# Performance work log

Hardware: AMD Instinct MI355X
Metric: run time of the kernel (lower is better)

## Reference

```python
import jax, jax.numpy as jnp
import numpy as np

N_NODES = 50000
N_EDGES = 800000
IN_DIM, HID, OUT = 128, 64, 64
NUM_REL = 2
LN_EPS = 1e-5


def setup_inputs() -> dict:
    key = jax.random.key(0)
    ks = jax.random.split(key, 16)
    inp = {
        "x": jax.random.normal(ks[0], (N_NODES, IN_DIM), dtype=jnp.float32),
        "edge_index": jax.random.randint(ks[1], (2, N_EDGES), 0, N_NODES, dtype=jnp.int64),
        "edge_type": jax.random.randint(ks[2], (N_EDGES,), 0, NUM_REL, dtype=jnp.int64),
        # layer 1 params (RGCNConv input->hidden + LayerNorm)
        "W1": jax.random.normal(ks[3], (NUM_REL, IN_DIM, HID), dtype=jnp.float32) * 0.05,
        "root1": jax.random.normal(ks[4], (IN_DIM, HID), dtype=jnp.float32) * 0.05,
        "b1": jnp.zeros((HID,), dtype=jnp.float32),
        "g1": jnp.ones((HID,), dtype=jnp.float32),
        "beta1": jnp.zeros((HID,), dtype=jnp.float32),
        # layer 2 params (RGCNConv hidden->output + LayerNorm)
        "W2": jax.random.normal(ks[5], (NUM_REL, HID, OUT), dtype=jnp.float32) * 0.05,
        "root2": jax.random.normal(ks[6], (HID, OUT), dtype=jnp.float32) * 0.05,
        "b2": jnp.zeros((OUT,), dtype=jnp.float32),
        "g2": jnp.ones((OUT,), dtype=jnp.float32),
        "beta2": jnp.zeros((OUT,), dtype=jnp.float32),
    }
    return inp


def rgcn_conv(x, W, root, bias, src, dst, edge_type, num_nodes):
    # PyG RGCNConv (aggr='mean'): out = x @ root + bias + sum_r mean_{j in N_r(i)} x_j @ W_r
    out = x @ root + bias
    for r in range(NUM_REL):
        mask = (edge_type == r).astype(x.dtype)        # [E]
        proj = x @ W[r]                                 # [N, out]
        msg = proj[src] * mask[:, None]                 # [E, out] gather + mask
        agg = jax.ops.segment_sum(msg, dst, num_segments=num_nodes)   # scatter-add
        cnt = jax.ops.segment_sum(mask, dst, num_segments=num_nodes)  # per-relation in-degree
        out = out + agg / jnp.maximum(cnt, 1.0)[:, None]
    return out


def layer_norm(x, g, b):
    mu = jnp.mean(x, axis=-1, keepdims=True)
    var = jnp.mean(jnp.square(x - mu), axis=-1, keepdims=True)
    return (x - mu) * jax.lax.rsqrt(var + LN_EPS) * g + b


def reference(x, edge_index, edge_type, W1, root1, b1, g1, beta1, W2, root2, b2, g2, beta2):
    src, dst = edge_index[0], edge_index[1]
    h = rgcn_conv(x, W1, root1, b1, src, dst, edge_type, x.shape[0])
    h = layer_norm(h, g1, beta1)
    h = jax.nn.gelu(h, approximate=False)  # dropout is identity in eval mode
    h = rgcn_conv(h, W2, root2, b2, src, dst, edge_type, x.shape[0])
    h = layer_norm(h, g2, beta2)
    return h
```

## Files before the change

### kernel.cpp

```cpp
#include <hip/hip_runtime.h>
#include <hip/hip_bf16.h>
#include <math.h>

#define IN_DIM 128
#define HID 64
#define NREL 2

using f32x4 = __attribute__((ext_vector_type(4))) float;
using s16x8 = __attribute__((ext_vector_type(8))) short;

__device__ __forceinline__ short f2bf(float f) {
    unsigned u = __float_as_uint(f);
    unsigned r = (u + 0x7fffu + ((u >> 16) & 1u)) >> 16;
    return (short)r;
}
__device__ __forceinline__ float bf2f(short b) {
    return __uint_as_float(((unsigned)(unsigned short)b) << 16);
}

__global__ void zero_ints(int* p, int n) {
    int i = blockIdx.x * blockDim.x + threadIdx.x;
    if (i < n) p[i] = 0;
}

__global__ void count_edges(const int* __restrict__ et, const int* __restrict__ dst,
                            int* __restrict__ cnt, int E, int N) {
    int e = blockIdx.x * blockDim.x + threadIdx.x;
    if (e < E) {
        atomicAdd(&cnt[et[e] * N + dst[e]], 1);
    }
}

#define SCAN_T 256
#define SCAN_I 4
__global__ void scan_phase1(const int* __restrict__ in, int* __restrict__ excl,
                            int* __restrict__ bsum, int n) {
    __shared__ int sdata[SCAN_T];
    int b = blockIdx.x;
    int t = threadIdx.x;
    int base = b * SCAN_T * SCAN_I;
    int v[SCAN_I];
    int s = 0;
#pragma unroll
    for (int i = 0; i < SCAN_I; ++i) {
        int idx = base + t * SCAN_I + i;
        v[i] = (idx < n) ? in[idx] : 0;
        s += v[i];
    }
    sdata[t] = s;
    __syncthreads();
    for (int off = 1; off < SCAN_T; off <<= 1) {
        int x = (t >= off) ? sdata[t - off] : 0;
        __syncthreads();
        sdata[t] += x;
        __syncthreads();
    }
    int run = sdata[t] - s;
    if (bsum && t == SCAN_T - 1) bsum[b] = sdata[SCAN_T - 1];
#pragma unroll
    for (int i = 0; i < SCAN_I; ++i) {
        int idx = base + t * SCAN_I + i;
        if (idx < n) excl[idx] = run;
        run += v[i];
    }
}

__global__ void scan_phase3(const int* __restrict__ excl, const int* __restrict__ boff,
                            int* __restrict__ rowptr, int* __restrict__ cursor,
                            int n, int total) {
    int i = blockIdx.x * blockDim.x + threadIdx.x;
    if (i < n) {
        int v = excl[i] + boff[i / (SCAN_T * SCAN_I)];
        rowptr[i] = v;
        cursor[i] = v;
    }
    if (i == 0) rowptr[n] = total;
}

__global__ void fill_edges(const int* __restrict__ et, const int* __restrict__ src,
                           const int* __restrict__ dst, int* __restrict__ cursor,
                           int* __restrict__ col, int E, int N) {
    int e = blockIdx.x * blockDim.x + threadIdx.x;
    if (e < E) {
        int slot = atomicAdd(&cursor[et[e] * N + dst[e]], 1);
        col[slot] = src[e];
    }
}

__device__ __forceinline__ void repack_one(const float* Wa, const float* Wb,
                                           const float* Wr, short* Wf, int T,
                                           int idx) {
    int g = idx >> 9;
    int r = idx & 511;
    int lane = r >> 3;
    int j = r & 7;
    int part = g & 1;
    int ct = g >> 1;
    int t = ct % T;
    int c = ct / T;
    int col = c * 16 + (lane & 15);
    int k = t * 32 + ((lane >> 4) << 3) + j;
    const float* Wg = (col < 64) ? Wa : (col < 128) ? Wb : Wr;
    float v = Wg[(size_t)k * 64 + (col & 63)];
    short hi = f2bf(v);
    Wf[idx] = part ? f2bf(v - bf2f(hi)) : hi;
}

__global__ void repack_w_frag(const float* __restrict__ W1,
                              const float* __restrict__ root1,
                              const float* __restrict__ W2,
                              const float* __restrict__ root2,
                              short* __restrict__ Wf1, short* __restrict__ Wf2) {
    const int L1 = 12 * 4 * 2 * 512;
    const int L2 = 12 * 2 * 2 * 512;
    int tid = blockIdx.x * blockDim.x + threadIdx.x;
    if (tid < L1) {
        repack_one(W1, W1 + (size_t)IN_DIM * 64, root1, Wf1, 4, tid);
    } else if (tid < L1 + L2) {
        repack_one(W2, W2 + (size_t)HID * 64, root2, Wf2, 2, tid - L1);
    }
}

template <int K>
__global__ __launch_bounds__(256) void gemm_mfma(
    const float* __restrict__ X, const short* __restrict__ Wf,
    float* __restrict__ PA, float* __restrict__ PB, float* __restrict__ PR,
    int M) {
    constexpr int T = K / 32;
    const int lane = threadIdx.x & 63;
    const int wid = threadIdx.x >> 6;
    const int row0 = blockIdx.x * 32 + (wid >> 1) * 16;
    const int cbase = (wid & 1) * 6;

    int arow = row0 + (lane & 15);
    if (arow > M - 1) arow = M - 1;
    const float* xr = X + (size_t)arow * K + ((lane >> 4) << 3);
    const s16x8* WfV = (const s16x8*)Wf;

    float4 xa[T][2];
#pragma unroll
    for (int t = 0; t < T; ++t) {
        xa[t][0] = *reinterpret_cast<const float4*>(xr + t * 32);
        xa[t][1] = *reinterpret_cast<const float4*>(xr + t * 32 + 4);
    }
    s16x8 ah[T], al[T];
#pragma unroll
    for (int t = 0; t < T; ++t) {
        const float av[8] = {xa[t][0].x, xa[t][0].y, xa[t][0].z, xa[t][0].w,
                             xa[t][1].x, xa[t][1].y, xa[t][1].z, xa[t][1].w};
#pragma unroll
        for (int j = 0; j < 8; ++j) {
            short h = f2bf(av[j]);
            ah[t][j] = h;
            al[t][j] = f2bf(av[j] - bf2f(h));
        }
    }

    f32x4 acc[6];
#pragma unroll
    for (int c = 0; c < 6; ++c) acc[c] = (f32x4){0.f, 0.f, 0.f, 0.f};

    s16x8 bhA[T], blA[T], bhB[T], blB[T];

#define LOADB(H, L, CG)                                                       \
    {                                                                         \
        _Pragma("unroll") for (int t = 0; t < T; ++t) {                       \
            H[t] = WfV[(size_t)(((CG) * T + t) * 2 + 0) * 64 + lane];         \
            L[t] = WfV[(size_t)(((CG) * T + t) * 2 + 1) * 64 + lane];         \
        }                                                                     \
    }
#define DOMFMA(H, L, CI)                                                      \
    {                                                                         \
        _Pragma("unroll") for (int t = 0; t < T; ++t) {                       \
            acc[CI] = __builtin_amdgcn_mfma_f32_16x16x32_bf16(ah[t], H[t],    \
                                                              acc[CI], 0, 0, 0); \
            acc[CI] = __builtin_amdgcn_mfma_f32_16x16x32_bf16(al[t], H[t],    \
                                                              acc[CI], 0, 0, 0); \
            acc[CI] = __builtin_amdgcn_mfma_f32_16x16x32_bf16(ah[t], L[t],    \
                                                              acc[CI], 0, 0, 0); \
        }                                                                     \
    }

    LOADB(bhA, blA, cbase + 0);
    LOADB(bhB, blB, cbase + 1);
    DOMFMA(bhA, blA, 0);
    LOADB(bhA, blA, cbase + 2);
    DOMFMA(bhB, blB, 1);
    LOADB(bhB, blB, cbase + 3);
    DOMFMA(bhA, blA, 2);
    LOADB(bhA, blA, cbase + 4);
    DOMFMA(bhB, blB, 3);
    LOADB(bhB, blB, cbase + 5);
    DOMFMA(bhA, blA, 4);
    DOMFMA(bhB, blB, 5);

#undef LOADB
#undef DOMFMA

    const int drow = row0 + ((lane >> 4) << 2);
    const int dcol = lane & 15;
#pragma unroll
    for (int ci = 0; ci < 6; ++ci) {
        const int cg = cbase + ci;
        float* base = (cg < 4) ? PA : (cg < 8) ? PB : PR;
        const int cc = (cg & 3) * 16 + dcol;
#pragma unroll
        for (int q = 0; q < 4; ++q) {
            const int row = drow + q;
            if (row < M) base[(size_t)row * 64 + cc] = acc[ci][q];
        }
    }
}

__device__ __forceinline__ float4 shfl_xor_f4(float4 v, int m) {
    return make_float4(__shfl_xor(v.x, m), __shfl_xor(v.y, m),
                       __shfl_xor(v.z, m), __shfl_xor(v.w, m));
}

__global__ __launch_bounds__(256) void agg_ln_kernel(
    const float* __restrict__ PA, const float* __restrict__ PB,
    const float* __restrict__ PR,
    const int* __restrict__ rowptr, const int* __restrict__ col,
    const float* __restrict__ bias, const float* __restrict__ g,
    const float* __restrict__ beta,
    float* __restrict__ out, int N, int gelu) {
    const int t = threadIdx.x;
    const int lane = t & 63;
    const int sub = lane >> 4;
    const int c = lane & 15;
    const int node = blockIdx.x * 4 + (t >> 6);
    if (node >= N) return;

    float4 acc = *reinterpret_cast<const float4*>(PR + (size_t)node * 64 + c * 4);
    {
        float4 b4 = *reinterpret_cast<const float4*>(bias + c * 4);
        acc.x += b4.x; acc.y += b4.y; acc.z += b4.z; acc.w += b4.w;
    }

#pragma unroll
    for (int r = 0; r < 2; ++r) {
        const float* __restrict__ P = r ? PB : PA;
        const int beg = rowptr[r * N + node];
        const int end = rowptr[r * N + node + 1];
        float4 s0 = make_float4(0.f, 0.f, 0.f, 0.f);
        float4 s1 = make_float4(0.f, 0.f, 0.f, 0.f);
        for (int i = beg + sub; i < end; i += 8) {
            const float4 v0 =
                *reinterpret_cast<const float4*>(P + (size_t)col[i] * 64 + c * 4);
            s0.x += v0.x; s0.y += v0.y; s0.z += v0.z; s0.w += v0.w;
            const int j = i + 4;
            if (j < end) {
                const float4 v1 =
                    *reinterpret_cast<const float4*>(P + (size_t)col[j] * 64 + c * 4);
                s1.x += v1.x; s1.y += v1.y; s1.z += v1.z; s1.w += v1.w;
            }
        }
        s0.x += s1.x; s0.y += s1.y; s0.z += s1.z; s0.w += s1.w;
        float4 o = shfl_xor_f4(s0, 16);
        s0.x += o.x; s0.y += o.y; s0.z += o.z; s0.w += o.w;
        o = shfl_xor_f4(s0, 32);
        s0.x += o.x; s0.y += o.y; s0.z += o.z; s0.w += o.w;
        const int deg = end - beg;
        if (deg > 0) {
            const float inv = 1.f / (float)deg;
            acc.x += s0.x * inv; acc.y += s0.y * inv;
            acc.z += s0.z * inv; acc.w += s0.w * inv;
        }
    }

    float ps = acc.x + acc.y + acc.z + acc.w;
#pragma unroll
    for (int off = 1; off <= 8; off <<= 1) ps += __shfl_xor(ps, off);
    const float mu = ps * (1.f / 64.f);
    const float4 d = make_float4(acc.x - mu, acc.y - mu, acc.z - mu, acc.w - mu);
    float vs = d.x * d.x + d.y * d.y + d.z * d.z + d.w * d.w;
#pragma unroll
    for (int off = 1; off <= 8; off <<= 1) vs += __shfl_xor(vs, off);
    const float rstd = 1.f / sqrtf(vs * (1.f / 64.f) + 1e-5f);

    const float4 g4 = *reinterpret_cast<const float4*>(g + c * 4);
    const float4 be4 = *reinterpret_cast<const float4*>(beta + c * 4);
    float4 y;
    y.x = d.x * rstd * g4.x + be4.x;
    y.y = d.y * rstd * g4.y + be4.y;
    y.z = d.z * rstd * g4.z + be4.z;
    y.w = d.w * rstd * g4.w + be4.w;

    if (gelu) {
        y.x = 0.5f * y.x * (1.f + erff(y.x * 0.70710678118654752440f));
        y.y = 0.5f * y.y * (1.f + erff(y.y * 0.70710678118654752440f));
        y.z = 0.5f * y.z * (1.f + erff(y.z * 0.70710678118654752440f));
        y.w = 0.5f * y.w * (1.f + erff(y.w * 0.70710678118654752440f));
    }

    if (sub == 0)
        *reinterpret_cast<float4*>(out + (size_t)node * 64 + c * 4) = y;
}

extern "C" void kernel_launch(void* const* d_in, const int* in_sizes, int n_in,
                              void* d_out, int out_size, void* d_ws, size_t ws_size,
                              hipStream_t stream) {
    const float* x = (const float*)d_in[0];
    const int* ei = (const int*)d_in[1];
    const int* et = (const int*)d_in[2];
    const float* W1 = (const float*)d_in[3];
    const float* root1 = (const float*)d_in[4];
    const float* b1 = (const float*)d_in[5];
    const float* g1 = (const float*)d_in[6];
    const float* beta1 = (const float*)d_in[7];
    const float* W2 = (const float*)d_in[8];
    const float* root2 = (const float*)d_in[9];
    const float* b2 = (const float*)d_in[10];
    const float* g2 = (const float*)d_in[11];
    const float* beta2 = (const float*)d_in[12];

    const int E = in_sizes[2];
    const int N = in_sizes[0] / IN_DIM;
    const int nseg = NREL * N;

    const int WF1 = 12 * 4 * 2 * 512;
    const int WF2 = 12 * 2 * 2 * 512;

    short* Wf1 = (short*)d_ws;
    short* Wf2 = Wf1 + WF1;
    float* PA = (float*)(Wf2 + WF2);
    float* PB = PA + (size_t)N * 64;
    float* PR = PB + (size_t)N * 64;
    float* H  = PR + (size_t)N * 64;
    int* cnt    = (int*)(H + (size_t)N * 64);
    int* excl   = cnt + nseg;
    int* rowptr = excl + nseg;
    int* cursor = rowptr + nseg + 1;
    int* colA   = cursor + nseg;
    int* bsum   = colA + E;
    int* boff   = bsum + 256;

    const int* esrc = ei;
    const int* edst = ei + E;

    zero_ints<<<(nseg + 255) / 256, 256, 0, stream>>>(cnt, nseg);
    count_edges<<<(E + 255) / 256, 256, 0, stream>>>(et, edst, cnt, E, N);
    int nb = (nseg + SCAN_T * SCAN_I - 1) / (SCAN_T * SCAN_I);
    scan_phase1<<<nb, SCAN_T, 0, stream>>>(cnt, excl, bsum, nseg);
    scan_phase1<<<1, SCAN_T, 0, stream>>>(bsum, boff, nullptr, nb);
    scan_phase3<<<(nseg + 255) / 256, 256, 0, stream>>>(excl, boff, rowptr, cursor,
                                                        nseg, E);
    fill_edges<<<(E + 255) / 256, 256, 0, stream>>>(et, esrc, edst, cursor, colA, E, N);

    repack_w_frag<<<(WF1 + WF2 + 255) / 256, 256, 0, stream>>>(
        W1, root1, W2, root2, Wf1, Wf2);

    int gblocks = (N + 31) / 32;
    gemm_mfma<IN_DIM><<<gblocks, 256, 0, stream>>>(x, Wf1, PA, PB, PR, N);
    agg_ln_kernel<<<(N + 3) / 4, 256, 0, stream>>>(PA, PB, PR, rowptr, colA, b1, g1,
                                                   beta1, H, N, 1);

    gemm_mfma<HID><<<gblocks, 256, 0, stream>>>(H, Wf2, PA, PB, PR, N);
    agg_ln_kernel<<<(N + 3) / 4, 256, 0, stream>>>(PA, PB, PR, rowptr, colA, b2, g2,
                                                   beta2, (float*)d_out, N, 0);
}
```

Before: 298.4 us.

## Merge per-relation CSR into single per-node CSR with precomputed edge weights

Builds one CSR indexed by destination node alone instead of one per (relation, node). Each edge entry packs the row index into a concatenated projection buffer together with its 1/deg weight, so the aggregation kernel runs a single loop with FMAs instead of two relation loops and a per-relation normalisation. The gather loop is unrolled four ways, and the scan covers half as many segments. This adds 8-byte edge records, which doubles index traffic, and moves the degree lookup into fill_edges.

```diff
diff --git a/kernel.cpp b/kernel.cpp
--- a/kernel.cpp
+++ b/kernel.cpp
@@ -33,8 +33,8 @@
 
 #define SCAN_T 256
 #define SCAN_I 4
-__global__ void scan_phase1(const int* __restrict__ in, int* __restrict__ excl,
-                            int* __restrict__ bsum, int n) {
+__global__ void scan_phase1(const int* __restrict__ in, const int* __restrict__ in2,
+                            int* __restrict__ excl, int* __restrict__ bsum, int n) {
     __shared__ int sdata[SCAN_T];
     int b = blockIdx.x;
     int t = threadIdx.x;
@@ -44,7 +44,7 @@
 #pragma unroll
     for (int i = 0; i < SCAN_I; ++i) {
         int idx = base + t * SCAN_I + i;
-        v[i] = (idx < n) ? in[idx] : 0;
+        v[i] = (idx < n) ? (in2 ? in[idx] + in2[idx] : in[idx]) : 0;
         s += v[i];
     }
     sdata[t] = s;
@@ -78,12 +78,21 @@
 }
 
 __global__ void fill_edges(const int* __restrict__ et, const int* __restrict__ src,
-                           const int* __restrict__ dst, int* __restrict__ cursor,
-                           int* __restrict__ col, int E, int N) {
+                           const int* __restrict__ dst, const int* __restrict__ cnt2,
+                           int* __restrict__ cursor, int2* __restrict__ colw,
+                           int E, int N) {
     int e = blockIdx.x * blockDim.x + threadIdx.x;
     if (e < E) {
-        int slot = atomicAdd(&cursor[et[e] * N + dst[e]], 1);
-        col[slot] = src[e];
+        int d = dst[e];
+        int r = et[e];
+        int s = src[e];
+        int slot = atomicAdd(&cursor[d], 1);
+        int deg = cnt2[r * N + d];
+        float iw = 1.f / (float)deg;
+        unsigned long long v = (unsigned long long)(unsigned)(r * N + s) |
+                               ((unsigned long long)__float_as_uint(iw) << 32);
+        __hip_atomic_store((unsigned long long*)(colw + slot), v,
+                           __ATOMIC_RELAXED, __HIP_MEMORY_SCOPE_AGENT);
     }
 }
 
@@ -218,9 +227,10 @@
 }
 
 __global__ __launch_bounds__(256) void agg_ln_kernel(
-    const float* __restrict__ PA, const float* __restrict__ PB,
+    const float* __restrict__ Pcat,
     const float* __restrict__ PR,
-    const int* __restrict__ rowptr, const int* __restrict__ col,
+    const int* __restrict__ rowptr,
+    const int2* __restrict__ colw,
     const float* __restrict__ bias, const float* __restrict__ g,
     const float* __restrict__ beta,
     float* __restrict__ out, int N, int gelu) {
@@ -231,42 +241,59 @@
     const int node = blockIdx.x * 4 + (t >> 6);
     if (node >= N) return;
 
-    float4 acc = *reinterpret_cast<const float4*>(PR + (size_t)node * 64 + c * 4);
+    const int c4 = c * 4;
+    float4 acc = *reinterpret_cast<const float4*>(PR + (size_t)node * 64 + c4);
     {
-        float4 b4 = *reinterpret_cast<const float4*>(bias + c * 4);
+        float4 b4 = *reinterpret_cast<const float4*>(bias + c4);
         acc.x += b4.x; acc.y += b4.y; acc.z += b4.z; acc.w += b4.w;
     }
 
-#pragma unroll
-    for (int r = 0; r < 2; ++r) {
-        const float* __restrict__ P = r ? PB : PA;
-        const int beg = rowptr[r * N + node];
-        const int end = rowptr[r * N + node + 1];
-        float4 s0 = make_float4(0.f, 0.f, 0.f, 0.f);
-        float4 s1 = make_float4(0.f, 0.f, 0.f, 0.f);
-        for (int i = beg + sub; i < end; i += 8) {
-            const float4 v0 =
-                *reinterpret_cast<const float4*>(P + (size_t)col[i] * 64 + c * 4);
-            s0.x += v0.x; s0.y += v0.y; s0.z += v0.z; s0.w += v0.w;
-            const int j = i + 4;
-            if (j < end) {
-                const float4 v1 =
-                    *reinterpret_cast<const float4*>(P + (size_t)col[j] * 64 + c * 4);
-                s1.x += v1.x; s1.y += v1.y; s1.z += v1.z; s1.w += v1.w;
-            }
-        }
-        s0.x += s1.x; s0.y += s1.y; s0.z += s1.z; s0.w += s1.w;
-        float4 o = shfl_xor_f4(s0, 16);
-        s0.x += o.x; s0.y += o.y; s0.z += o.z; s0.w += o.w;
-        o = shfl_xor_f4(s0, 32);
-        s0.x += o.x; s0.y += o.y; s0.z += o.z; s0.w += o.w;
-        const int deg = end - beg;
-        if (deg > 0) {
-            const float inv = 1.f / (float)deg;
-            acc.x += s0.x * inv; acc.y += s0.y * inv;
-            acc.z += s0.z * inv; acc.w += s0.w * inv;
-        }
-    }
+    const int beg = rowptr[node];
+    const int end = rowptr[node + 1];
+    float4 s0 = make_float4(0.f, 0.f, 0.f, 0.f);
+    float4 s1 = s0, s2 = s0, s3 = s0;
+    for (int i = beg + sub; i < end; i += 16) {
+        {
+            const int2 w = colw[i];
+            const float4 v = *reinterpret_cast<const float4*>(Pcat + w.x * 64 + c4);
+            const float f = __int_as_float(w.y);
+            s0.x = fmaf(v.x, f, s0.x); s0.y = fmaf(v.y, f, s0.y);
+            s0.z = fmaf(v.z, f, s0.z); s0.w = fmaf(v.w, f, s0.w);
+        }
+        int j = i + 4;
+        if (j < end) {
+            const int2 w = colw[j];
+            const float4 v = *reinterpret_cast<const float4*>(Pcat + w.x * 64 + c4);
+            const float f = __int_as_float(w.y);
+            s1.x = fmaf(v.x, f, s1.x); s1.y = fmaf(v.y, f, s1.y);
+            s1.z = fmaf(v.z, f, s1.z); s1.w = fmaf(v.w, f, s1.w);
+        }
+        j = i + 8;
+        if (j < end) {
+            const int2 w = colw[j];
+            const float4 v = *reinterpret_cast<const float4*>(Pcat + w.x * 64 + c4);
+            const float f = __int_as_float(w.y);
+            s2.x = fmaf(v.x, f, s2.x); s2.y = fmaf(v.y, f, s2.y);
+            s2.z = fmaf(v.z, f, s2.z); s2.w = fmaf(v.w, f, s2.w);
+        }
+        j = i + 12;
+        if (j < end) {
+            const int2 w = colw[j];
+            const float4 v = *reinterpret_cast<const float4*>(Pcat + w.x * 64 + c4);
+            const float f = __int_as_float(w.y);
+            s3.x = fmaf(v.x, f, s3.x); s3.y = fmaf(v.y, f, s3.y);
+            s3.z = fmaf(v.z, f, s3.z); s3.w = fmaf(v.w, f, s3.w);
+        }
+    }
+    s0.x += s1.x + s2.x + s3.x;
+    s0.y += s1.y + s2.y + s3.y;
+    s0.z += s1.z + s2.z + s3.z;
+    s0.w += s1.w + s2.w + s3.w;
+    float4 o = shfl_xor_f4(s0, 16);
+    s0.x += o.x; s0.y += o.y; s0.z += o.z; s0.w += o.w;
+    o = shfl_xor_f4(s0, 32);
+    s0.x += o.x; s0.y += o.y; s0.z += o.z; s0.w += o.w;
+    acc.x += s0.x; acc.y += s0.y; acc.z += s0.z; acc.w += s0.w;
 
     float ps = acc.x + acc.y + acc.z + acc.w;
 #pragma unroll
@@ -278,8 +305,8 @@
     for (int off = 1; off <= 8; off <<= 1) vs += __shfl_xor(vs, off);
     const float rstd = 1.f / sqrtf(vs * (1.f / 64.f) + 1e-5f);
 
-    const float4 g4 = *reinterpret_cast<const float4*>(g + c * 4);
-    const float4 be4 = *reinterpret_cast<const float4*>(beta + c * 4);
+    const float4 g4 = *reinterpret_cast<const float4*>(g + c4);
+    const float4 be4 = *reinterpret_cast<const float4*>(beta + c4);
     float4 y;
     y.x = d.x * rstd * g4.x + be4.x;
     y.y = d.y * rstd * g4.y + be4.y;
@@ -294,7 +321,7 @@
     }
 
     if (sub == 0)
-        *reinterpret_cast<float4*>(out + (size_t)node * 64 + c * 4) = y;
+        *reinterpret_cast<float4*>(out + (size_t)node * 64 + c4) = y;
 }
 
 extern "C" void kernel_launch(void* const* d_in, const int* in_sizes, int n_in,
@@ -316,46 +343,46 @@
 
     const int E = in_sizes[2];
     const int N = in_sizes[0] / IN_DIM;
-    const int nseg = NREL * N;
 
     const int WF1 = 12 * 4 * 2 * 512;
     const int WF2 = 12 * 2 * 2 * 512;
 
     short* Wf1 = (short*)d_ws;
     short* Wf2 = Wf1 + WF1;
-    float* PA = (float*)(Wf2 + WF2);
-    float* PB = PA + (size_t)N * 64;
-    float* PR = PB + (size_t)N * 64;
-    float* H  = PR + (size_t)N * 64;
-    int* cnt    = (int*)(H + (size_t)N * 64);
-    int* excl   = cnt + nseg;
-    int* rowptr = excl + nseg;
-    int* cursor = rowptr + nseg + 1;
-    int* colA   = cursor + nseg;
-    int* bsum   = colA + E;
+    float* Pcat = (float*)(Wf2 + WF2);
+    float* PR   = Pcat + (size_t)2 * N * 64;
+    float* H    = PR + (size_t)N * 64;
+    int2* colw  = (int2*)(H + (size_t)N * 64);
+    int* cnt2   = (int*)(colw + E);
+    int* excl   = cnt2 + 2 * N;
+    int* rowptr = excl + N;
+    int* cursor = rowptr + N + 1;
+    int* bsum   = cursor + N;
     int* boff   = bsum + 256;
 
     const int* esrc = ei;
     const int* edst = ei + E;
 
-    zero_ints<<<(nseg + 255) / 256, 256, 0, stream>>>(cnt, nseg);
-    count_edges<<<(E + 255) / 256, 256, 0, stream>>>(et, edst, cnt, E, N);
-    int nb = (nseg + SCAN_T * SCAN_I - 1) / (SCAN_T * SCAN_I);
-    scan_phase1<<<nb, SCAN_T, 0, stream>>>(cnt, excl, bsum, nseg);
-    scan_phase1<<<1, SCAN_T, 0, stream>>>(bsum, boff, nullptr, nb);
-    scan_phase3<<<(nseg + 255) / 256, 256, 0, stream>>>(excl, boff, rowptr, cursor,
-                                                        nseg, E);
-    fill_edges<<<(E + 255) / 256, 256, 0, stream>>>(et, esrc, edst, cursor, colA, E, N);
+    zero_ints<<<(2 * N + 255) / 256, 256, 0, stream>>>(cnt2, 2 * N);
+    count_edges<<<(E + 255) / 256, 256, 0, stream>>>(et, edst, cnt2, E, N);
+    int nb = (N + SCAN_T * SCAN_I - 1) / (SCAN_T * SCAN_I);
+    scan_phase1<<<nb, SCAN_T, 0, stream>>>(cnt2, cnt2 + N, excl, bsum, N);
+    scan_phase1<<<1, SCAN_T, 0, stream>>>(bsum, nullptr, boff, nullptr, nb);
+    scan_phase3<<<(N + 255) / 256, 256, 0, stream>>>(excl, boff, rowptr, cursor, N, E);
+    fill_edges<<<(E + 255) / 256, 256, 0, stream>>>(et, esrc, edst, cnt2, cursor,
+                                                    colw, E, N);
 
     repack_w_frag<<<(WF1 + WF2 + 255) / 256, 256, 0, stream>>>(
         W1, root1, W2, root2, Wf1, Wf2);
 
     int gblocks = (N + 31) / 32;
-    gemm_mfma<IN_DIM><<<gblocks, 256, 0, stream>>>(x, Wf1, PA, PB, PR, N);
-    agg_ln_kernel<<<(N + 3) / 4, 256, 0, stream>>>(PA, PB, PR, rowptr, colA, b1, g1,
+    gemm_mfma<IN_DIM><<<gblocks, 256, 0, stream>>>(
+        x, Wf1, Pcat, Pcat + (size_t)N * 64, PR, N);
+    agg_ln_kernel<<<(N + 3) / 4, 256, 0, stream>>>(Pcat, PR, rowptr, colw, b1, g1,
                                                    beta1, H, N, 1);
 
-    gemm_mfma<HID><<<gblocks, 256, 0, stream>>>(H, Wf2, PA, PB, PR, N);
-    agg_ln_kernel<<<(N + 3) / 4, 256, 0, stream>>>(PA, PB, PR, rowptr, colA, b2, g2,
+    gemm_mfma<HID><<<gblocks, 256, 0, stream>>>(
+        H, Wf2, Pcat, Pcat + (size_t)N * 64, PR, N);
+    agg_ln_kernel<<<(N + 3) / 4, 256, 0, stream>>>(Pcat, PR, rowptr, colw, b2, g2,
                                                    beta2, (float*)d_out, N, 0);
 }
```

New measurement: 290.3 us. -2.7%, faster.
